# Optimization experiments

Hardware: AMD Instinct MI355X
Metric: run time of the kernel (lower is better)

Reference implementation:

```python
import jax, jax.numpy as jnp
import numpy as np


def setup_inputs() -> dict:
    key = jax.random.key(0)
    k1, k2, k3, k4, k5 = jax.random.split(key, 5)
    B, S, DIN, DOUT = 4, 4096, 1024, 4096
    input_ = jax.random.normal(k1, (B, S, DIN), dtype=jnp.float32)
    weights = jax.random.normal(k2, (DOUT, DIN), dtype=jnp.float32) * 0.02
    # two cluster centroids (each shape (1,), as produced by kmeans.cluster_centers_[k])
    c1 = jax.random.uniform(k3, (1,), dtype=jnp.float32) * 0.02
    c2 = -jax.random.uniform(k4, (1,), dtype=jnp.float32) * 0.02
    bias = jax.random.normal(k5, (DOUT,), dtype=jnp.float32) * 0.02
    return {"input_": input_, "weights": weights, "c1": c1, "c2": c2, "bias": bias}


def reference(input_, weights, c1, c2, bias):
    # upper = max(c1, c2), lower = min(c1, c2), threshold = upper - lower
    upper = jnp.maximum(c1, c2)  # (1,)
    lower = jnp.minimum(c1, c2)  # (1,)
    middle = upper - lower       # (1,)
    # binarize weights: w < middle -> lower, else -> upper (fused with GEMM downstream)
    w = jnp.where(weights < middle, lower, upper)  # [DOUT, DIN]
    # F.linear: input @ w.T + bias
    out = jnp.einsum("bsi,oi->bso", input_, w) + bias
    return out
```

## Files before the change

### kernel.cpp

```cpp
#include <hip/hip_runtime.h>
#include <hip/hip_bf16.h>


typedef __bf16 bf16x8 __attribute__((ext_vector_type(8)));
typedef float  f32x4  __attribute__((ext_vector_type(4)));

__device__ inline unsigned short f2bf(float f) {
    unsigned int u = __float_as_uint(f);
    u += 0x7FFFu + ((u >> 16) & 1u);
    return (unsigned short)(u >> 16);
}

__global__ void cvt_x_kernel(const float4* __restrict__ in,
                             ushort4* __restrict__ out, int n4) {
    int stride = gridDim.x * blockDim.x;
    for (int i = blockIdx.x * blockDim.x + threadIdx.x; i < n4; i += stride) {
        float4 v = in[i];
        ushort4 o;
        o.x = f2bf(v.x); o.y = f2bf(v.y); o.z = f2bf(v.z); o.w = f2bf(v.w);
        out[i] = o;
    }
}

__global__ void bin_w_kernel(const float4* __restrict__ w,
                             ushort4* __restrict__ out,
                             const float* __restrict__ c1,
                             const float* __restrict__ c2, int n4) {
    const float a = c1[0], b = c2[0];
    const float upper  = fmaxf(a, b);
    const float lower  = fminf(a, b);
    const float middle = upper - lower;
    const unsigned short lo16 = f2bf(lower);
    const unsigned short up16 = f2bf(upper);
    int stride = gridDim.x * blockDim.x;
    for (int i = blockIdx.x * blockDim.x + threadIdx.x; i < n4; i += stride) {
        float4 v = w[i];
        ushort4 o;
        o.x = (v.x < middle) ? lo16 : up16;
        o.y = (v.y < middle) ? lo16 : up16;
        o.z = (v.z < middle) ? lo16 : up16;
        o.w = (v.w < middle) ? lo16 : up16;
        out[i] = o;
    }
}

__device__ inline void async16(void* lds, const void* g) {
    __builtin_amdgcn_global_load_lds(
        (const __attribute__((address_space(1))) void*)g,
        (__attribute__((address_space(3))) void*)lds,
        16, 0, 0);
}

__global__ __launch_bounds__(256) void gemm_bin(
        const ushort* __restrict__ A,
        const ushort* __restrict__ B,
        const float*  __restrict__ bias,
        float* __restrict__ C,
        int M, int N, int K) {
    __shared__ ushort As[128 * 32];
    __shared__ ushort Bs[128 * 32];

    const int tid  = threadIdx.x;
    const int wave = tid >> 6;
    const int lane = tid & 63;

    const int bn = blockIdx.x;
    const int bm = blockIdx.y;
    const int row0 = bm * 128;
    const int col0 = bn * 128;

    const int wm = (wave & 1) * 64;
    const int wn = (wave >> 1) * 64;

    f32x4 acc[4][4];
#pragma unroll
    for (int i = 0; i < 4; ++i)
#pragma unroll
        for (int j = 0; j < 4; ++j)
            acc[i][j] = (f32x4){0.f, 0.f, 0.f, 0.f};

    const int sr = tid >> 2;
    const int sc = (tid & 3) * 8;
    const ushort* a0 = A + (size_t)(row0 + sr) * K + sc;
    const ushort* a1 = A + (size_t)(row0 + 64 + sr) * K + sc;
    const ushort* b0 = B + (size_t)(col0 + sr) * K + sc;
    const ushort* b1 = B + (size_t)(col0 + 64 + sr) * K + sc;

    ushort* asd0 = &As[wave * 512];
    ushort* asd1 = &As[2048 + wave * 512];
    ushort* bsd0 = &Bs[wave * 512];
    ushort* bsd1 = &Bs[2048 + wave * 512];

    const int fr = lane & 15;
    const int fk = (lane >> 4) * 8;

    for (int k0 = 0; k0 < K; k0 += 32) {
        async16(asd0, a0 + k0);
        async16(asd1, a1 + k0);
        async16(bsd0, b0 + k0);
        async16(bsd1, b1 + k0);
        __syncthreads();

        bf16x8 af[4], bf[4];
#pragma unroll
        for (int i = 0; i < 4; ++i)
            af[i] = *(const bf16x8*)&As[(wm + i * 16 + fr) * 32 + fk];
#pragma unroll
        for (int j = 0; j < 4; ++j)
            bf[j] = *(const bf16x8*)&Bs[(wn + j * 16 + fr) * 32 + fk];

#pragma unroll
        for (int i = 0; i < 4; ++i)
#pragma unroll
            for (int j = 0; j < 4; ++j)
                acc[i][j] = __builtin_amdgcn_mfma_f32_16x16x32_bf16(
                    af[i], bf[j], acc[i][j], 0, 0, 0);

        __syncthreads();
    }

    const int er = (lane >> 4) * 4;
    const int ec = lane & 15;
#pragma unroll
    for (int j = 0; j < 4; ++j) {
        const int col = col0 + wn + j * 16 + ec;
        const float bz = bias[col];
#pragma unroll
        for (int i = 0; i < 4; ++i) {
            const size_t rbase = (size_t)(row0 + wm + i * 16 + er) * N + col;
#pragma unroll
            for (int r = 0; r < 4; ++r)
                C[rbase + (size_t)r * N] = acc[i][j][r] + bz;
        }
    }
}

extern "C" void kernel_launch(void* const* d_in, const int* in_sizes, int n_in,
                              void* d_out, int out_size, void* d_ws, size_t ws_size,
                              hipStream_t stream) {
    const float* x    = (const float*)d_in[0];
    const float* w    = (const float*)d_in[1];
    const float* c1   = (const float*)d_in[2];
    const float* c2   = (const float*)d_in[3];
    const float* bias = (const float*)d_in[4];
    float* out = (float*)d_out;

    const int DOUT = in_sizes[4];
    const int DIN  = in_sizes[1] / DOUT;
    const int M    = in_sizes[0] / DIN;
    const int N    = DOUT;
    const int K    = DIN;

    ushort* xb = (ushort*)d_ws;
    ushort* wb = xb + (size_t)M * K;

    const int nx4 = (M * K) / 4;
    const int nw4 = (N * K) / 4;
    cvt_x_kernel<<<4096, 256, 0, stream>>>((const float4*)x, (ushort4*)xb, nx4);
    bin_w_kernel<<<1024, 256, 0, stream>>>((const float4*)w, (ushort4*)wb, c1, c2, nw4);

    dim3 grid(N / 128, M / 128);
    gemm_bin<<<grid, 256, 0, stream>>>(xb, wb, bias, out, M, N, K);
}
```

Measured before the change: 477.1 us.

## Switch GEMM to 32x32x16 MFMA with XOR-swizzled LDS layout

Replaces the 4x4 grid of 16x16x32 bf16 MFMAs per wave with a 2x2 grid of 32x32x16 MFMAs over two k-halves, and XOR-swizzles the 8-element column chunks when staging tiles into LDS so fragment reads avoid bank conflicts. The larger MFMA shape needs fewer fragment loads per FLOP, and the swizzle targets LDS bank conflicts on the strided row reads. The epilogue is rewritten for the 32x32 accumulator layout. The kernel still uses a single LDS buffer with two barriers per k-step, so global-load latency is still not overlapped.

Result: slower. 491.3 us (+3.0%).

```diff
diff --git a/kernel.cpp b/kernel.cpp
--- a/kernel.cpp
+++ b/kernel.cpp
@@ -3,7 +3,7 @@
 
 
 typedef __bf16 bf16x8 __attribute__((ext_vector_type(8)));
-typedef float  f32x4  __attribute__((ext_vector_type(4)));
+typedef float  f32x16 __attribute__((ext_vector_type(16)));
 
 __device__ inline unsigned short f2bf(float f) {
     unsigned int u = __float_as_uint(f);
@@ -63,6 +63,8 @@
     const int tid  = threadIdx.x;
     const int wave = tid >> 6;
     const int lane = tid & 63;
+    const int l31  = lane & 31;
+    const int lhi  = lane >> 5;
 
     const int bn = blockIdx.x;
     const int bm = blockIdx.y;
@@ -72,15 +74,18 @@
     const int wm = (wave & 1) * 64;
     const int wn = (wave >> 1) * 64;
 
-    f32x4 acc[4][4];
+    f32x16 acc[2][2];
 #pragma unroll
-    for (int i = 0; i < 4; ++i)
+    for (int i = 0; i < 2; ++i)
 #pragma unroll
-        for (int j = 0; j < 4; ++j)
-            acc[i][j] = (f32x4){0.f, 0.f, 0.f, 0.f};
+        for (int j = 0; j < 2; ++j)
+#pragma unroll
+            for (int r = 0; r < 16; ++r)
+                acc[i][j][r] = 0.f;
 
     const int sr = tid >> 2;
-    const int sc = (tid & 3) * 8;
+    const int sq = (tid & 3) ^ ((sr >> 1) & 3);
+    const int sc = sq * 8;
     const ushort* a0 = A + (size_t)(row0 + sr) * K + sc;
     const ushort* a1 = A + (size_t)(row0 + 64 + sr) * K + sc;
     const ushort* b0 = B + (size_t)(col0 + sr) * K + sc;
@@ -91,8 +96,9 @@
     ushort* bsd0 = &Bs[wave * 512];
     ushort* bsd1 = &Bs[2048 + wave * 512];
 
-    const int fr = lane & 15;
-    const int fk = (lane >> 4) * 8;
+    const int sKey  = (l31 >> 1) & 3;
+    const int aHalf = (wm >> 6) * 2048;
+    const int bHalf = (wn >> 6) * 2048;
 
     for (int k0 = 0; k0 < K; k0 += 32) {
         async16(asd0, a0 + k0);
@@ -101,36 +107,43 @@
         async16(bsd1, b1 + k0);
         __syncthreads();
 
-        bf16x8 af[4], bf[4];
+        bf16x8 af[2][2], bfr[2][2];
 #pragma unroll
-        for (int i = 0; i < 4; ++i)
-            af[i] = *(const bf16x8*)&As[(wm + i * 16 + fr) * 32 + fk];
+        for (int h = 0; h < 2; ++h) {
+            const int q  = (h << 1) | lhi;
+            const int co = ((q ^ sKey) << 3);
 #pragma unroll
-        for (int j = 0; j < 4; ++j)
-            bf[j] = *(const bf16x8*)&Bs[(wn + j * 16 + fr) * 32 + fk];
+            for (int i = 0; i < 2; ++i)
+                af[i][h] = *(const bf16x8*)&As[aHalf + (i * 32 + l31) * 32 + co];
+#pragma unroll
+            for (int j = 0; j < 2; ++j)
+                bfr[j][h] = *(const bf16x8*)&Bs[bHalf + (j * 32 + l31) * 32 + co];
+        }
 
 #pragma unroll
-        for (int i = 0; i < 4; ++i)
+        for (int h = 0; h < 2; ++h)
 #pragma unroll
-            for (int j = 0; j < 4; ++j)
-                acc[i][j] = __builtin_amdgcn_mfma_f32_16x16x32_bf16(
-                    af[i], bf[j], acc[i][j], 0, 0, 0);
+            for (int i = 0; i < 2; ++i)
+#pragma unroll
+                for (int j = 0; j < 2; ++j)
+                    acc[i][j] = __builtin_amdgcn_mfma_f32_32x32x16_bf16(
+                        af[i][h], bfr[j][h], acc[i][j], 0, 0, 0);
 
         __syncthreads();
     }
 
-    const int er = (lane >> 4) * 4;
-    const int ec = lane & 15;
 #pragma unroll
-    for (int j = 0; j < 4; ++j) {
-        const int col = col0 + wn + j * 16 + ec;
+    for (int j = 0; j < 2; ++j) {
+        const int col = col0 + wn + j * 32 + l31;
         const float bz = bias[col];
 #pragma unroll
-        for (int i = 0; i < 4; ++i) {
-            const size_t rbase = (size_t)(row0 + wm + i * 16 + er) * N + col;
+        for (int i = 0; i < 2; ++i) {
+            const int rbase = row0 + wm + i * 32 + 4 * lhi;
 #pragma unroll
-            for (int r = 0; r < 4; ++r)
-                C[rbase + (size_t)r * N] = acc[i][j][r] + bz;
+            for (int reg = 0; reg < 16; ++reg) {
+                const int row = rbase + (reg & 3) + 8 * (reg >> 2);
+                C[(size_t)row * N + col] = acc[i][j][reg] + bz;
+            }
         }
     }
 }
```
